# Optimization experiments

Measured on AMD Instinct MI355X. Metric: run time of the kernel, lower is better.

Reference implementation:

```python
import jax, jax.numpy as jnp
import numpy as np

S = 128          # voxel grid resolution per axis
NPB = 50000      # active voxels per batch element
B = 2            # batch size
C_IN = 64
C_OUT = 64
K = 3            # kernel size

# kernel offsets in [-1,0,1]^3, shape [27, 3]
_OFFS = np.stack(np.meshgrid(np.arange(-1, 2), np.arange(-1, 2), np.arange(-1, 2), indexing='ij'), axis=-1).reshape(-1, 3)


def setup_inputs() -> dict:
    rng = np.random.default_rng(0)
    coords_list = []
    for b in range(B):
        lin = rng.choice(S * S * S, size=NPB, replace=False)  # unique voxels
        x = lin // (S * S)
        y = (lin // S) % S
        z = lin % S
        coords_list.append(np.stack([np.full(NPB, b), x, y, z], axis=1))
    coords = jnp.asarray(np.concatenate(coords_list, axis=0), dtype=jnp.int32)  # [N,4]

    key = jax.random.key(0)
    k1, k2, k3 = jax.random.split(key, 3)
    feats = jax.random.normal(k1, (B * NPB, C_IN), dtype=jnp.float32)
    fan1 = C_IN * K ** 3
    fan2 = C_OUT * K ** 3
    W1 = jax.random.normal(k2, (K ** 3, C_IN, C_OUT), dtype=jnp.float32) / np.sqrt(fan1)
    W2 = jax.random.normal(k3, (K ** 3, C_OUT, C_OUT), dtype=jnp.float32) / np.sqrt(fan2)
    return {"feats": feats, "coords": coords, "W1": W1, "W2": W2}


def _encode(coords):
    # linear key: ((b*S + x)*S + y)*S + z ; fits in int32 for S=128, B small
    b, x, y, z = coords[:, 0], coords[:, 1], coords[:, 2], coords[:, 3]
    return ((b * S + x) * S + y) * S + z


def _sparse_conv(feats, coords, W):
    """Stride-1 sparse (submanifold-style) 3D conv: output coords == input coords.
    feats [N,Cin], coords [N,4], W [27,Cin,Cout] -> [N,Cout]."""
    N = feats.shape[0]
    keys = _encode(coords)
    order = jnp.argsort(keys)
    skeys = keys[order]
    offs = jnp.asarray(_OFFS, dtype=jnp.int32)  # [27,3]

    def gather_one(d):
        qxyz = coords[:, 1:4] + d[None, :]
        valid = jnp.all((qxyz >= 0) & (qxyz < S), axis=1)
        qkey = keys + (d[0] * S * S + d[1] * S + d[2])
        idx = jnp.clip(jnp.searchsorted(skeys, qkey), 0, N - 1)
        found = valid & (skeys[idx] == qkey)
        return jnp.where(found[:, None], feats[order[idx]], 0.0)  # [N,Cin]

    gathered = jax.vmap(gather_one)(offs)  # [27, N, Cin]
    return jnp.einsum('onc,ocd->nd', gathered, W)


def reference(feats, coords, W1, W2):
    h = _sparse_conv(feats, coords, W1)
    out = _sparse_conv(h, coords, W2)
    return out
```

## Files before the change

### kernel.cpp

```cpp
#include <hip/hip_runtime.h>
#include <stdint.h>

#define SGRID 128
#define CAP 4096

typedef _Float16 f16;
typedef f16 f16x8 __attribute__((ext_vector_type(8)));
typedef float f32x4 __attribute__((ext_vector_type(4)));
typedef unsigned long long u64;

static __device__ __forceinline__ f32x4 mfma16(uint4 a, uint4 b, f32x4 c) {
    union { uint4 u; f16x8 v; } ua, ub;
    ua.u = a; ub.u = b;
    return __builtin_amdgcn_mfma_f32_16x16x32_f16(ua.v, ub.v, c, 0, 0, 0);
}

static __device__ __forceinline__ void split8(const float* v, uint4& hu, uint4& lu) {
    union { f16 h[8]; uint4 u; } hv, lv;
    #pragma unroll
    for (int j = 0; j < 8; ++j) {
        f16 h = (f16)v[j];
        hv.h[j] = h;
        lv.h[j] = (f16)(v[j] - (float)h);
    }
    hu = hv.u; lu = lv.u;
}

static __device__ __forceinline__ void center_tail(
    const float* __restrict__ A, const uint4 b[2][4],
    float* __restrict__ O, int N, int gw, int lane)
{
    const int r = lane & 15, lq = lane >> 4;
    const int p0 = gw * 32;

    uint4 ah[2][2], al[2][2];
    #pragma unroll
    for (int rt = 0; rt < 2; ++rt) {
        int row = p0 + rt * 16 + r;
        #pragma unroll
        for (int ks = 0; ks < 2; ++ks) {
            float v[8];
            if (row < N) {
                float4 v0 = *(const float4*)(A + (size_t)row * 64 + ks * 32 + lq * 8);
                float4 v1 = *(const float4*)(A + (size_t)row * 64 + ks * 32 + lq * 8 + 4);
                v[0]=v0.x; v[1]=v0.y; v[2]=v0.z; v[3]=v0.w;
                v[4]=v1.x; v[5]=v1.y; v[6]=v1.z; v[7]=v1.w;
            } else {
                #pragma unroll
                for (int j = 0; j < 8; ++j) v[j] = 0.f;
            }
            split8(v, ah[rt][ks], al[rt][ks]);
        }
    }

    f32x4 acc[2][4];
    #pragma unroll
    for (int i = 0; i < 2; ++i)
        #pragma unroll
        for (int j = 0; j < 4; ++j) acc[i][j] = (f32x4){0.f, 0.f, 0.f, 0.f};

    #pragma unroll
    for (int ks = 0; ks < 2; ++ks)
        #pragma unroll
        for (int rt = 0; rt < 2; ++rt)
            #pragma unroll
            for (int ct = 0; ct < 4; ++ct) {
                acc[rt][ct] = mfma16(ah[rt][ks], b[ks][ct], acc[rt][ct]);
                acc[rt][ct] = mfma16(al[rt][ks], b[ks][ct], acc[rt][ct]);
            }

    #pragma unroll
    for (int rt = 0; rt < 2; ++rt)
        #pragma unroll
        for (int j = 0; j < 4; ++j) {
            int row = p0 + rt * 16 + lq * 4 + j;
            if (row < N) {
                #pragma unroll
                for (int ct = 0; ct < 4; ++ct)
                    O[(size_t)row * 64 + ct * 16 + r] = acc[rt][ct][j];
            }
        }
}

__global__ void clear_meta(uint4* __restrict__ bitmap4, int nwords4, int* __restrict__ cnt) {
    const int stride = gridDim.x * 256;
    for (int i = blockIdx.x * 256 + threadIdx.x; i < nwords4; i += stride)
        bitmap4[i] = (uint4){0, 0, 0, 0};
    if (blockIdx.x == 0 && threadIdx.x < 26) cnt[threadIdx.x * 16] = 0;
}

__global__ void __launch_bounds__(256) prep_center(
    const float* __restrict__ F, const float* __restrict__ W1, float* __restrict__ H,
    const int* __restrict__ coords, int* __restrict__ table, unsigned* __restrict__ bitmap,
    const float* __restrict__ W2, f16* __restrict__ Wp1, f16* __restrict__ Wp2,
    int N, int centerB, int scatB)
{
    const int tid = threadIdx.x;
    int bid = blockIdx.x;

    if (bid < centerB) {
        int gw = (bid * 256 + tid) >> 6;
        if (gw >= (N + 31) >> 5) return;
        const int lane = tid & 63, r = lane & 15, lq = lane >> 4;
        const float* Wc = W1 + 13 * 4096;
        uint4 b[2][4];
        #pragma unroll
        for (int ct = 0; ct < 4; ++ct) {
            int co = ct * 16 + r;
            #pragma unroll
            for (int ks = 0; ks < 2; ++ks) {
                int ci0 = ks * 32 + lq * 8;
                union { f16 h[8]; uint4 u; } hv;
                #pragma unroll
                for (int j = 0; j < 8; ++j)
                    hv.h[j] = (f16)Wc[(ci0 + j) * 64 + co];
                b[ks][ct] = hv.u;
            }
        }
        center_tail(F, b, H, N, gw, lane);
        return;
    }
    bid -= centerB;

    if (bid < scatB) {
        int i = bid * 256 + tid;
        if (i < N) {
            int4 c = ((const int4*)coords)[i];
            int key = ((c.x * SGRID + c.y) * SGRID + c.z) * SGRID + c.w;
            table[key] = i;
            atomicOr(&bitmap[key >> 5], 1u << (key & 31));
        }
        return;
    }
    bid -= scatB;

    {
        int idx = bid * 256 + tid;
        const int half = 27 * 512;
        const float* W = (idx < half) ? W1 : W2;
        f16* Wp = (idx < half) ? Wp1 : Wp2;
        int id = (idx < half) ? idx : idx - half;
        int lane = id & 63;
        int ks = (id >> 6) & 1;
        int ct = (id >> 7) & 3;
        int o  = id >> 9;
        int co  = ct * 16 + (lane & 15);
        int ci0 = ks * 32 + (lane >> 4) * 8;
        union { f16 h[8]; uint4 u; } hv;
        #pragma unroll
        for (int j = 0; j < 8; ++j)
            hv.h[j] = (f16)W[((size_t)o * 64 + ci0 + j) * 64 + co];
        ((uint4*)Wp)[id] = hv.u;
    }
}

__global__ void __launch_bounds__(256) build(
    const int* __restrict__ coords, const int* __restrict__ table,
    const unsigned* __restrict__ bitmap,
    int* __restrict__ pin, int* __restrict__ pout, int* __restrict__ cnt, int N)
{
    __shared__ u64 sbal[26][4];
    __shared__ int sbase4[26][4];

    const int tid = threadIdx.x, lane = tid & 63, wave = tid >> 6;
    const int n = blockIdx.x * 256 + tid;
    const bool valid = n < N;

    int4 c = {0, 0, 0, 0};
    if (valid) c = ((const int4*)coords)[n];
    const int z  = c.w;
    const int zb = (z == 0) ? 0 : z - 1;
    const int wofs = zb >> 5, sh = zb & 31;

    unsigned omask = 0;
    #pragma unroll
    for (int cidx = 0; cidx < 9; ++cidx) {
        int dx = cidx / 3 - 1, dy = cidx % 3 - 1;
        int qx = c.y + dx, qy = c.z + dy;
        bool colok = valid && ((unsigned)qx < SGRID) && ((unsigned)qy < SGRID);
        int wi = colok ? ((((c.x * SGRID + qx) * SGRID + qy) << 2) + wofs) : 0;
        unsigned w0 = bitmap[wi];
        unsigned w1 = bitmap[wi + 1];
        u64 w = (u64)w0 | ((u64)w1 << 32);
        unsigned t = (unsigned)(w >> sh) & 7u;
        if (z == 0)         t = (t << 1) & 6u;
        if (z == SGRID - 1) t &= 3u;
        t = colok ? t : 0u;
        omask |= t << (cidx * 3);
    }
    omask &= ~(1u << 13);

    const int key = ((c.x * SGRID + c.y) * SGRID + c.z) * SGRID + z;
    int nb[26];
    #pragma unroll
    for (int s = 0; s < 26; ++s) {
        int o = s < 13 ? s : s + 1;
        bool occ = (omask >> o) & 1u;
        int qkey = key + (o / 9 - 1) * SGRID * SGRID + ((o / 3) % 3 - 1) * SGRID + (o % 3 - 1);
        int v = table[occ ? qkey : 0];
        nb[s] = occ ? v : -1;
    }

    #pragma unroll
    for (int s = 0; s < 26; ++s) {
        u64 bal = __ballot(nb[s] >= 0);
        if (lane == 0) sbal[s][wave] = bal;
    }
    __syncthreads();

    if (tid < 26) {
        int c0 = (int)__popcll(sbal[tid][0]);
        int c1 = (int)__popcll(sbal[tid][1]);
        int c2 = (int)__popcll(sbal[tid][2]);
        int c3 = (int)__popcll(sbal[tid][3]);
        int tot = c0 + c1 + c2 + c3;
        int base = tot ? atomicAdd(&cnt[tid * 16], tot) : 0;
        sbase4[tid][0] = base;
        sbase4[tid][1] = base + c0;
        sbase4[tid][2] = base + c0 + c1;
        sbase4[tid][3] = base + c0 + c1 + c2;
    }
    __syncthreads();

    const u64 ltmask = (1ull << lane) - 1ull;
    #pragma unroll
    for (int s = 0; s < 26; ++s) {
        if (nb[s] >= 0) {
            int pos = sbase4[s][wave] + (int)__popcll(sbal[s][wave] & ltmask);
            if (pos < CAP) {
                pin[s * CAP + pos]  = nb[s];
                pout[s * CAP + pos] = n;
            }
        }
    }
}

__global__ void __launch_bounds__(256) conv_center(
    const float* __restrict__ A, const f16* __restrict__ Wp,
    float* __restrict__ O, int N)
{
    int gw = (blockIdx.x * 256 + threadIdx.x) >> 6;
    if (gw >= (N + 31) >> 5) return;
    const int lane = threadIdx.x & 63;
    const uint4* wb = (const uint4*)Wp + 13 * 512 + lane;
    uint4 b[2][4];
    #pragma unroll
    for (int ct = 0; ct < 4; ++ct)
        #pragma unroll
        for (int ks = 0; ks < 2; ++ks)
            b[ks][ct] = wb[(ct * 2 + ks) * 64];
    center_tail(A, b, O, N, gw, lane);
}

__global__ void __launch_bounds__(256) conv_sparse(
    const float* __restrict__ A, const f16* __restrict__ Wp,
    const int* __restrict__ pin, const int* __restrict__ pout,
    const int* __restrict__ cnt, float* __restrict__ O)
{
    int w = (blockIdx.x * 256 + threadIdx.x) >> 6;
    if (w >= 26 * 512) return;
    int slot  = w >> 9;
    int rem   = w & 511;
    int chunk = rem >> 1;
    int ch    = rem & 1;
    int cn = cnt[slot * 16]; if (cn > CAP) cn = CAP;
    int i0 = chunk * 16;
    if (i0 >= cn) return;
    int o = slot < 13 ? slot : slot + 1;
    const int lane = threadIdx.x & 63, r = lane & 15, lq = lane >> 4;

    const uint4* wb = (const uint4*)Wp + (size_t)o * 512 + lane;
    uint4 b[2][2];
    #pragma unroll
    for (int ct = 0; ct < 2; ++ct)
        #pragma unroll
        for (int ks = 0; ks < 2; ++ks)
            b[ct][ks] = wb[((ch * 2 + ct) * 2 + ks) * 64];

    int p = i0 + r;
    int in = (p < cn) ? pin[slot * CAP + p] : -1;
    uint4 ah[2], al[2];
    #pragma unroll
    for (int ks = 0; ks < 2; ++ks) {
        float v[8];
        if (in >= 0) {
            float4 v0 = *(const float4*)(A + (size_t)in * 64 + ks * 32 + lq * 8);
            float4 v1 = *(const float4*)(A + (size_t)in * 64 + ks * 32 + lq * 8 + 4);
            v[0]=v0.x; v[1]=v0.y; v[2]=v0.z; v[3]=v0.w;
            v[4]=v1.x; v[5]=v1.y; v[6]=v1.z; v[7]=v1.w;
        } else {
            #pragma unroll
            for (int j = 0; j < 8; ++j) v[j] = 0.f;
        }
        split8(v, ah[ks], al[ks]);
    }

    f32x4 acc[2];
    acc[0] = (f32x4){0.f, 0.f, 0.f, 0.f};
    acc[1] = (f32x4){0.f, 0.f, 0.f, 0.f};
    #pragma unroll
    for (int ks = 0; ks < 2; ++ks)
        #pragma unroll
        for (int ct = 0; ct < 2; ++ct) {
            acc[ct] = mfma16(ah[ks], b[ct][ks], acc[ct]);
            acc[ct] = mfma16(al[ks], b[ct][ks], acc[ct]);
        }

    #pragma unroll
    for (int j = 0; j < 4; ++j) {
        int pr = i0 + lq * 4 + j;
        if (pr < cn) {
            int oidx = pout[slot * CAP + pr];
            #pragma unroll
            for (int ct = 0; ct < 2; ++ct)
                atomicAdd(&O[(size_t)oidx * 64 + (ch * 2 + ct) * 16 + r], acc[ct][j]);
        }
    }
}

extern "C" void kernel_launch(void* const* d_in, const int* in_sizes, int n_in,
                              void* d_out, int out_size, void* d_ws, size_t ws_size,
                              hipStream_t stream) {
    const float* feats  = (const float*)d_in[0];
    const int*   coords = (const int*)d_in[1];
    const float* W1     = (const float*)d_in[2];
    const float* W2     = (const float*)d_in[3];
    float* out = (float*)d_out;

    const int N = in_sizes[0] / 64;
    const size_t nvox = 2ull * SGRID * SGRID * SGRID;

    char* p = (char*)d_ws;
    int*      table  = (int*)p;      p += nvox * 4;
    unsigned* bitmap = (unsigned*)p; p += (nvox / 32) * 4;
    p += 16;
    int*      cnt    = (int*)p;      p += 26 * 16 * 4;
    int*      pin    = (int*)p;      p += 26ull * CAP * 4;
    int*      pout   = (int*)p;      p += 26ull * CAP * 4;
    float*    H      = (float*)p;    p += (size_t)N * 64 * 4;
    f16*      Wp1    = (f16*)p;      p += 27ull * 4096 * 2;
    f16*      Wp2    = (f16*)p;      p += 27ull * 4096 * 2;

    const int bm4     = (int)(nvox / 32 / 4) + 1;
    const int scatB   = (N + 255) / 256;
    const int ngroups = (N + 31) / 32;
    const int centerB = (ngroups + 3) / 4;
    const int sparseB = 26 * 512 / 4;

    clear_meta<<<256, 256, 0, stream>>>((uint4*)bitmap, bm4, cnt);
    prep_center<<<centerB + scatB + 108, 256, 0, stream>>>(
        feats, W1, H, coords, table, bitmap, W2, Wp1, Wp2, N, centerB, scatB);
    build<<<scatB, 256, 0, stream>>>(coords, table, bitmap, pin, pout, cnt, N);
    conv_sparse<<<sparseB, 256, 0, stream>>>(feats, Wp1, pin, pout, cnt, H);
    conv_center<<<centerB, 256, 0, stream>>>(H, Wp2, out, N);
    conv_sparse<<<sparseB, 256, 0, stream>>>(H, Wp2, pin, pout, cnt, out);
}
```

Measured before the change: 99.26 us.

## Stage feature rows through LDS with async global_load_lds and fuse center conv into build

```diff
diff --git a/kernel.cpp b/kernel.cpp
--- a/kernel.cpp
+++ b/kernel.cpp
@@ -26,32 +26,53 @@
     hu = hv.u; lu = lv.u;
 }
 
-static __device__ __forceinline__ void center_tail(
-    const float* __restrict__ A, const uint4 b[2][4],
-    float* __restrict__ O, int N, int gw, int lane)
-{
+static __device__ __forceinline__ void gload16(const void* g, void* l) {
+    __builtin_amdgcn_global_load_lds(
+        (const __attribute__((address_space(1))) unsigned int*)g,
+        (__attribute__((address_space(3))) unsigned int*)l, 16, 0, 0);
+}
+
+static __device__ __forceinline__ void read_row_frags(
+    const float* __restrict__ sW, int rl, int lq, uint4 ah[2], uint4 al[2])
+{
+    #pragma unroll
+    for (int ks = 0; ks < 2; ++ks) {
+        int c0 = ks * 8 + lq * 2;
+        int s0 = (c0 - rl) & 15, s1 = (c0 + 1 - rl) & 15;
+        float4 v0 = *(const float4*)&sW[(rl * 16 + s0) * 4];
+        float4 v1 = *(const float4*)&sW[(rl * 16 + s1) * 4];
+        float v[8] = {v0.x, v0.y, v0.z, v0.w, v1.x, v1.y, v1.z, v1.w};
+        split8(v, ah[ks], al[ks]);
+    }
+}
+
+static __device__ __forceinline__ void center_staged(
+    const float* __restrict__ A, const uint4 b[2][4], float* __restrict__ O,
+    int N, int gw0, int tid, float* sF)
+{
+    const int w = tid >> 6, lane = tid & 63;
     const int r = lane & 15, lq = lane >> 4;
+    const int gw = gw0 + w;
     const int p0 = gw * 32;
+    float* sW = sF + w * 2048;
+
+    #pragma unroll
+    for (int j = 0; j < 8; ++j) {
+        int ch = j * 64 + lane;
+        int rl = ch >> 4, slot = ch & 15;
+        int csrc = (slot + rl) & 15;
+        int grow = p0 + rl;
+        if (grow > N - 1) grow = N - 1;
+        gload16(A + (size_t)grow * 64 + csrc * 4, sW + j * 256);
+    }
+    asm volatile("s_waitcnt vmcnt(0)" ::: "memory");
+    __builtin_amdgcn_sched_barrier(0);
+    if (p0 >= N) return;
 
     uint4 ah[2][2], al[2][2];
     #pragma unroll
-    for (int rt = 0; rt < 2; ++rt) {
-        int row = p0 + rt * 16 + r;
-        #pragma unroll
-        for (int ks = 0; ks < 2; ++ks) {
-            float v[8];
-            if (row < N) {
-                float4 v0 = *(const float4*)(A + (size_t)row * 64 + ks * 32 + lq * 8);
-                float4 v1 = *(const float4*)(A + (size_t)row * 64 + ks * 32 + lq * 8 + 4);
-                v[0]=v0.x; v[1]=v0.y; v[2]=v0.z; v[3]=v0.w;
-                v[4]=v1.x; v[5]=v1.y; v[6]=v1.z; v[7]=v1.w;
-            } else {
-                #pragma unroll
-                for (int j = 0; j < 8; ++j) v[j] = 0.f;
-            }
-            split8(v, ah[rt][ks], al[rt][ks]);
-        }
-    }
+    for (int rt = 0; rt < 2; ++rt)
+        read_row_frags(sW, rt * 16 + r, lq, ah[rt], al[rt]);
 
     f32x4 acc[2][4];
     #pragma unroll
@@ -82,88 +103,14 @@
         }
 }
 
-__global__ void clear_meta(uint4* __restrict__ bitmap4, int nwords4, int* __restrict__ cnt) {
-    const int stride = gridDim.x * 256;
-    for (int i = blockIdx.x * 256 + threadIdx.x; i < nwords4; i += stride)
-        bitmap4[i] = (uint4){0, 0, 0, 0};
-    if (blockIdx.x == 0 && threadIdx.x < 26) cnt[threadIdx.x * 16] = 0;
-}
-
-__global__ void __launch_bounds__(256) prep_center(
-    const float* __restrict__ F, const float* __restrict__ W1, float* __restrict__ H,
-    const int* __restrict__ coords, int* __restrict__ table, unsigned* __restrict__ bitmap,
-    const float* __restrict__ W2, f16* __restrict__ Wp1, f16* __restrict__ Wp2,
-    int N, int centerB, int scatB)
-{
-    const int tid = threadIdx.x;
-    int bid = blockIdx.x;
-
-    if (bid < centerB) {
-        int gw = (bid * 256 + tid) >> 6;
-        if (gw >= (N + 31) >> 5) return;
-        const int lane = tid & 63, r = lane & 15, lq = lane >> 4;
-        const float* Wc = W1 + 13 * 4096;
-        uint4 b[2][4];
-        #pragma unroll
-        for (int ct = 0; ct < 4; ++ct) {
-            int co = ct * 16 + r;
-            #pragma unroll
-            for (int ks = 0; ks < 2; ++ks) {
-                int ci0 = ks * 32 + lq * 8;
-                union { f16 h[8]; uint4 u; } hv;
-                #pragma unroll
-                for (int j = 0; j < 8; ++j)
-                    hv.h[j] = (f16)Wc[(ci0 + j) * 64 + co];
-                b[ks][ct] = hv.u;
-            }
-        }
-        center_tail(F, b, H, N, gw, lane);
-        return;
-    }
-    bid -= centerB;
-
-    if (bid < scatB) {
-        int i = bid * 256 + tid;
-        if (i < N) {
-            int4 c = ((const int4*)coords)[i];
-            int key = ((c.x * SGRID + c.y) * SGRID + c.z) * SGRID + c.w;
-            table[key] = i;
-            atomicOr(&bitmap[key >> 5], 1u << (key & 31));
-        }
-        return;
-    }
-    bid -= scatB;
-
-    {
-        int idx = bid * 256 + tid;
-        const int half = 27 * 512;
-        const float* W = (idx < half) ? W1 : W2;
-        f16* Wp = (idx < half) ? Wp1 : Wp2;
-        int id = (idx < half) ? idx : idx - half;
-        int lane = id & 63;
-        int ks = (id >> 6) & 1;
-        int ct = (id >> 7) & 3;
-        int o  = id >> 9;
-        int co  = ct * 16 + (lane & 15);
-        int ci0 = ks * 32 + (lane >> 4) * 8;
-        union { f16 h[8]; uint4 u; } hv;
-        #pragma unroll
-        for (int j = 0; j < 8; ++j)
-            hv.h[j] = (f16)W[((size_t)o * 64 + ci0 + j) * 64 + co];
-        ((uint4*)Wp)[id] = hv.u;
-    }
-}
-
-__global__ void __launch_bounds__(256) build(
+static __device__ __forceinline__ void build_body(
     const int* __restrict__ coords, const int* __restrict__ table,
     const unsigned* __restrict__ bitmap,
-    int* __restrict__ pin, int* __restrict__ pout, int* __restrict__ cnt, int N)
-{
-    __shared__ u64 sbal[26][4];
-    __shared__ int sbase4[26][4];
-
-    const int tid = threadIdx.x, lane = tid & 63, wave = tid >> 6;
-    const int n = blockIdx.x * 256 + tid;
+    int* __restrict__ pin, int* __restrict__ pout, int* __restrict__ cnt,
+    int N, int ck, int tid, u64 (*sbal)[4], int (*sbase4)[4])
+{
+    const int lane = tid & 63, wave = tid >> 6;
+    const int n = ck * 256 + tid;
     const bool valid = n < N;
 
     int4 c = {0, 0, 0, 0};
@@ -235,12 +182,89 @@
     }
 }
 
+static __device__ __forceinline__ void wprep_item(
+    const float* __restrict__ W1, const float* __restrict__ W2,
+    f16* __restrict__ Wp1, f16* __restrict__ Wp2, int idx)
+{
+    const int half = 27 * 512;
+    const float* W = (idx < half) ? W1 : W2;
+    f16* Wp = (idx < half) ? Wp1 : Wp2;
+    int id = (idx < half) ? idx : idx - half;
+    int lane = id & 63;
+    int ks = (id >> 6) & 1;
+    int ct = (id >> 7) & 3;
+    int o  = id >> 9;
+    int co  = ct * 16 + (lane & 15);
+    int ci0 = ks * 32 + (lane >> 4) * 8;
+    union { f16 h[8]; uint4 u; } hv;
+    #pragma unroll
+    for (int j = 0; j < 8; ++j)
+        hv.h[j] = (f16)W[((size_t)o * 64 + ci0 + j) * 64 + co];
+    ((uint4*)Wp)[id] = hv.u;
+}
+
+__global__ void clear_meta(uint4* __restrict__ bitmap4, int nwords4,
+                           int* __restrict__ cnt, float* __restrict__ zrow) {
+    const int stride = gridDim.x * 256;
+    for (int i = blockIdx.x * 256 + threadIdx.x; i < nwords4; i += stride)
+        bitmap4[i] = (uint4){0, 0, 0, 0};
+    if (blockIdx.x == 0 && threadIdx.x < 26) cnt[threadIdx.x * 16] = 0;
+    if (blockIdx.x == 0 && threadIdx.x < 64) zrow[threadIdx.x] = 0.f;
+}
+
+__global__ void __launch_bounds__(256) scatter_prep(
+    const int* __restrict__ coords, int* __restrict__ table,
+    unsigned* __restrict__ bitmap, int N, int scatB,
+    const float* __restrict__ W1, const float* __restrict__ W2,
+    f16* __restrict__ Wp1, f16* __restrict__ Wp2)
+{
+    const int tid = threadIdx.x;
+    if (blockIdx.x < scatB) {
+        int i = blockIdx.x * 256 + tid;
+        if (i < N) {
+            int4 c = ((const int4*)coords)[i];
+            int key = ((c.x * SGRID + c.y) * SGRID + c.z) * SGRID + c.w;
+            table[key] = i;
+            atomicOr(&bitmap[key >> 5], 1u << (key & 31));
+        }
+        return;
+    }
+    wprep_item(W1, W2, Wp1, Wp2, (blockIdx.x - scatB) * 256 + tid);
+}
+
+__global__ void __launch_bounds__(256) build_center(
+    const int* __restrict__ coords, const int* __restrict__ table,
+    const unsigned* __restrict__ bitmap,
+    int* __restrict__ pin, int* __restrict__ pout, int* __restrict__ cnt,
+    int N, int probeB,
+    const float* __restrict__ F, const f16* __restrict__ Wp, float* __restrict__ H)
+{
+    __shared__ union {
+        float sF[8192];
+        struct { u64 sbal[26][4]; int sbase4[26][4]; } pb;
+    } sm;
+
+    if (blockIdx.x >= probeB) {
+        const int lane = threadIdx.x & 63;
+        const uint4* wb = (const uint4*)Wp + 13 * 512 + lane;
+        uint4 b[2][4];
+        #pragma unroll
+        for (int ct = 0; ct < 4; ++ct)
+            #pragma unroll
+            for (int ks = 0; ks < 2; ++ks)
+                b[ks][ct] = wb[(ct * 2 + ks) * 64];
+        center_staged(F, b, H, N, (blockIdx.x - probeB) * 4, threadIdx.x, sm.sF);
+        return;
+    }
+    build_body(coords, table, bitmap, pin, pout, cnt, N, blockIdx.x, threadIdx.x,
+               sm.pb.sbal, sm.pb.sbase4);
+}
+
 __global__ void __launch_bounds__(256) conv_center(
     const float* __restrict__ A, const f16* __restrict__ Wp,
     float* __restrict__ O, int N)
 {
-    int gw = (blockIdx.x * 256 + threadIdx.x) >> 6;
-    if (gw >= (N + 31) >> 5) return;
+    __shared__ float sF[8192];
     const int lane = threadIdx.x & 63;
     const uint4* wb = (const uint4*)Wp + 13 * 512 + lane;
     uint4 b[2][4];
@@ -249,16 +273,20 @@
         #pragma unroll
         for (int ks = 0; ks < 2; ++ks)
             b[ks][ct] = wb[(ct * 2 + ks) * 64];
-    center_tail(A, b, O, N, gw, lane);
+    center_staged(A, b, O, N, blockIdx.x * 4, threadIdx.x, sF);
 }
 
 __global__ void __launch_bounds__(256) conv_sparse(
     const float* __restrict__ A, const f16* __restrict__ Wp,
     const int* __restrict__ pin, const int* __restrict__ pout,
-    const int* __restrict__ cnt, float* __restrict__ O)
-{
+    const int* __restrict__ cnt, float* __restrict__ O,
+    const float* __restrict__ zrow)
+{
+    __shared__ float sF[4096];
     int w = (blockIdx.x * 256 + threadIdx.x) >> 6;
     if (w >= 26 * 512) return;
+    const int lane = threadIdx.x & 63;
+    const int wv = threadIdx.x >> 6;
     int slot  = w >> 9;
     int rem   = w & 511;
     int chunk = rem >> 1;
@@ -267,7 +295,24 @@
     int i0 = chunk * 16;
     if (i0 >= cn) return;
     int o = slot < 13 ? slot : slot + 1;
-    const int lane = threadIdx.x & 63, r = lane & 15, lq = lane >> 4;
+    const int r = lane & 15, lq = lane >> 4;
+    float* sW = sF + wv * 1024;
+
+    #pragma unroll
+    for (int i = 0; i < 4; ++i) {
+        int rl = i * 4 + (lane >> 4);
+        int slotc = lane & 15;
+        int csrc = (slotc + rl) & 15;
+        int p = i0 + rl;
+        const float* src;
+        if (p < cn) {
+            int rid = pin[slot * CAP + p];
+            src = A + (size_t)rid * 64 + csrc * 4;
+        } else {
+            src = zrow + csrc * 4;
+        }
+        gload16(src, sW + i * 256);
+    }
 
     const uint4* wb = (const uint4*)Wp + (size_t)o * 512 + lane;
     uint4 b[2][2];
@@ -277,23 +322,11 @@
         for (int ks = 0; ks < 2; ++ks)
             b[ct][ks] = wb[((ch * 2 + ct) * 2 + ks) * 64];
 
-    int p = i0 + r;
-    int in = (p < cn) ? pin[slot * CAP + p] : -1;
+    asm volatile("s_waitcnt vmcnt(0)" ::: "memory");
+    __builtin_amdgcn_sched_barrier(0);
+
     uint4 ah[2], al[2];
-    #pragma unroll
-    for (int ks = 0; ks < 2; ++ks) {
-        float v[8];
-        if (in >= 0) {
-            float4 v0 = *(const float4*)(A + (size_t)in * 64 + ks * 32 + lq * 8);
-            float4 v1 = *(const float4*)(A + (size_t)in * 64 + ks * 32 + lq * 8 + 4);
-            v[0]=v0.x; v[1]=v0.y; v[2]=v0.z; v[3]=v0.w;
-            v[4]=v1.x; v[5]=v1.y; v[6]=v1.z; v[7]=v1.w;
-        } else {
-            #pragma unroll
-            for (int j = 0; j < 8; ++j) v[j] = 0.f;
-        }
-        split8(v, ah[ks], al[ks]);
-    }
+    read_row_frags(sW, r, lq, ah, al);
 
     f32x4 acc[2];
     acc[0] = (f32x4){0.f, 0.f, 0.f, 0.f};
@@ -335,6 +368,7 @@
     unsigned* bitmap = (unsigned*)p; p += (nvox / 32) * 4;
     p += 16;
     int*      cnt    = (int*)p;      p += 26 * 16 * 4;
+    float*    zrow   = (float*)p;    p += 64 * 4;
     int*      pin    = (int*)p;      p += 26ull * CAP * 4;
     int*      pout   = (int*)p;      p += 26ull * CAP * 4;
     float*    H      = (float*)p;    p += (size_t)N * 64 * 4;
@@ -347,11 +381,13 @@
     const int centerB = (ngroups + 3) / 4;
     const int sparseB = 26 * 512 / 4;
 
-    clear_meta<<<256, 256, 0, stream>>>((uint4*)bitmap, bm4, cnt);
-    prep_center<<<centerB + scatB + 108, 256, 0, stream>>>(
-        feats, W1, H, coords, table, bitmap, W2, Wp1, Wp2, N, centerB, scatB);
-    build<<<scatB, 256, 0, stream>>>(coords, table, bitmap, pin, pout, cnt, N);
-    conv_sparse<<<sparseB, 256, 0, stream>>>(feats, Wp1, pin, pout, cnt, H);
+    clear_meta<<<256, 256, 0, stream>>>((uint4*)bitmap, bm4, cnt, zrow);
+    scatter_prep<<<scatB + 108, 256, 0, stream>>>(coords, table, bitmap, N, scatB,
+                                                  W1, W2, Wp1, Wp2);
+    build_center<<<scatB + centerB, 256, 0, stream>>>(coords, table, bitmap,
+                                                      pin, pout, cnt, N, scatB,
+                                                      feats, Wp1, H);
+    conv_sparse<<<sparseB, 256, 0, stream>>>(feats, Wp1, pin, pout, cnt, H, zrow);
     conv_center<<<centerB, 256, 0, stream>>>(H, Wp2, out, N);
-    conv_sparse<<<sparseB, 256, 0, stream>>>(H, Wp2, pin, pout, cnt, out);
-}
+    conv_sparse<<<sparseB, 256, 0, stream>>>(H, Wp2, pin, pout, cnt, out, zrow);
+}
```

Result: faster. 95.05 us (-4.2%).
